# Kernel optimization log

Hardware: AMD Instinct MI355X
Metric: run time of the kernel (lower is better)

The kernel has to match this reference:

```python
import jax, jax.numpy as jnp
import numpy as np
from jax import lax

B, T, EPROJS, DUNITS, ATT_DIM = 32, 2048, 1024, 1024, 512
ACONV_CHANS, ACONV_FILTS = 32, 15
SCALING = 2.0


def setup_inputs() -> dict:
    key = jax.random.key(0)
    ks = jax.random.split(key, 12)
    enc_hs_pad = jax.random.normal(ks[0], (B, T, EPROJS), dtype=jnp.float32)
    enc_hs_len = jax.random.randint(ks[1], (B,), T // 2, T + 1, dtype=jnp.int32)
    dec_z = jax.random.normal(ks[2], (B, DUNITS), dtype=jnp.float32)
    ap = jax.random.uniform(ks[3], (B, T), dtype=jnp.float32)
    att_prev = ap / jnp.sum(ap, axis=1, keepdims=True)  # previous attention distribution
    # parameters (PyTorch Linear: y = x @ W^T + b; stored here pre-transposed as [in, out])
    s_enc = 1.0 / np.sqrt(EPROJS)
    s_dec = 1.0 / np.sqrt(DUNITS)
    s_att = 1.0 / np.sqrt(ACONV_CHANS)
    s_g = 1.0 / np.sqrt(ATT_DIM)
    K = 2 * ACONV_FILTS + 1
    s_c = 1.0 / np.sqrt(K)
    W_enc = jax.random.uniform(ks[4], (EPROJS, ATT_DIM), jnp.float32, -s_enc, s_enc)
    b_enc = jax.random.uniform(ks[5], (ATT_DIM,), jnp.float32, -s_enc, s_enc)
    W_dec = jax.random.uniform(ks[6], (DUNITS, ATT_DIM), jnp.float32, -s_dec, s_dec)
    W_att = jax.random.uniform(ks[7], (ACONV_CHANS, ATT_DIM), jnp.float32, -s_att, s_att)
    conv_w = jax.random.uniform(ks[8], (ACONV_CHANS, 1, K), jnp.float32, -s_c, s_c)
    W_g = jax.random.uniform(ks[9], (ATT_DIM, 1), jnp.float32, -s_g, s_g)
    b_g = jax.random.uniform(ks[10], (1,), jnp.float32, -s_g, s_g)
    return {"enc_hs_pad": enc_hs_pad, "enc_hs_len": enc_hs_len, "dec_z": dec_z,
            "att_prev": att_prev, "W_enc": W_enc, "b_enc": b_enc, "W_dec": W_dec,
            "W_att": W_att, "conv_w": conv_w, "W_g": W_g, "b_g": b_g}


def reference(enc_hs_pad, enc_hs_len, dec_z, att_prev,
              W_enc, b_enc, W_dec, W_att, conv_w, W_g, b_g):
    # pre-computed encoder projection: (B, T, A)
    pre_enc = jnp.einsum('btd,da->bta', enc_hs_pad, W_enc) + b_enc
    # location conv over previous attention: (B, 1, T) -> (B, C, T), SAME padding
    pad = (conv_w.shape[-1] - 1) // 2
    att_conv = lax.conv_general_dilated(
        att_prev[:, None, :], conv_w, window_strides=(1,),
        padding=[(pad, pad)], dimension_numbers=('NCH', 'OIH', 'NCH'))
    att_c = jnp.einsum('bct,ca->bta', att_conv, W_att)       # (B, T, A)
    dec_t = (dec_z @ W_dec)[:, None, :]                       # (B, 1, A)
    # energies: (B, T)
    e = jnp.einsum('bta,ao->bt', jnp.tanh(att_c + pre_enc + dec_t), W_g) + b_g[0]
    # pad mask: True where t >= length
    mask = jnp.arange(e.shape[1])[None, :] >= enc_hs_len[:, None]
    e = jnp.where(mask, -jnp.inf, e)
    w = jax.nn.softmax(SCALING * e, axis=1)                   # (B, T)
    c = jnp.einsum('btd,bt->bd', enc_hs_pad, w)               # (B, EPROJS)
    return c, w
```

## Files before the change

### kernel.cpp

```cpp
#include <hip/hip_runtime.h>
#include <stdint.h>

#define T_LEN 2048
#define KAUG  1056
#define M_TOT 65536

typedef __attribute__((ext_vector_type(8))) short short8;
typedef __attribute__((ext_vector_type(4))) float f32x4;
typedef unsigned int u32;
typedef unsigned short u16;

__device__ __forceinline__ u16 bf16_rn(float f){
  u32 u = __builtin_bit_cast(u32, f);
  u32 r = u + 0x7fffu + ((u >> 16) & 1u);
  return (u16)(r >> 16);
}
__device__ __forceinline__ u32 pack_trunc(float lo, float hi){
  u32 a = __builtin_bit_cast(u32, lo);
  u32 b = __builtin_bit_cast(u32, hi);
  return (a >> 16) | (b & 0xffff0000u);
}

__global__ void k_build_bt(const float* __restrict__ W_enc,
                           const float* __restrict__ W_att,
                           u16* __restrict__ Bt){
  __shared__ float tile[32][33];
  int k0 = blockIdx.x * 32, n0 = blockIdx.y * 32;
  int tx = threadIdx.x & 31, ty = threadIdx.x >> 5;
  #pragma unroll
  for (int i = 0; i < 4; i++){
    int k = k0 + i*8 + ty;
    int n = n0 + tx;
    float v = (k < 1024) ? W_enc[k*512 + n] : W_att[(k-1024)*512 + n];
    tile[i*8+ty][tx] = v;
  }
  __syncthreads();
  #pragma unroll
  for (int i = 0; i < 4; i++){
    int n = n0 + i*8 + ty;
    int k = k0 + tx;
    Bt[(size_t)n*KAUG + k] = bf16_rn(tile[tx][i*8+ty]);
  }
}

__global__ void k_bias(const float* __restrict__ dec_z,
                       const float* __restrict__ W_dec,
                       const float* __restrict__ b_enc,
                       float* __restrict__ bias){
  __shared__ float red[4][64];
  int b = blockIdx.y, n0 = blockIdx.x * 64;
  int nl = threadIdx.x & 63, ks = threadIdx.x >> 6;
  int n = n0 + nl;
  const float* dz = dec_z + b*1024;
  float s = 0.f;
  #pragma unroll 4
  for (int k = ks*256; k < ks*256 + 256; k++) s += dz[k] * W_dec[k*512 + n];
  red[ks][nl] = s;
  __syncthreads();
  if (threadIdx.x < 64){
    int nn = n0 + threadIdx.x;
    bias[b*512 + nn] = b_enc[nn] + red[0][threadIdx.x] + red[1][threadIdx.x]
                     + red[2][threadIdx.x] + red[3][threadIdx.x];
  }
}

__global__ void k_conv(const float* __restrict__ att_prev,
                       const float* __restrict__ conv_w,
                       float* __restrict__ attT){
  int idx = blockIdx.x*256 + threadIdx.x;
  int c = idx & 31;
  int bt = idx >> 5;
  int b = bt >> 11, t = bt & 2047;
  const float* ap = att_prev + b*2048;
  const float* cw = conv_w + c*31;
  float s = 0.f;
  #pragma unroll
  for (int j = 0; j < 31; j++){
    int tt = t + j - 15;
    float a = (tt >= 0 && tt < 2048) ? ap[tt] : 0.f;
    s += cw[j] * a;
  }
  attT[(size_t)bt*32 + c] = s;
}

__launch_bounds__(256, 3)
__global__ void k_gemm_energy(const float* __restrict__ enc,
                              const float* __restrict__ attT,
                              const u16* __restrict__ Bt,
                              const float* __restrict__ bias,
                              const float* __restrict__ Wg,
                              float* __restrict__ ePart){
  __shared__ __align__(16) u16 Ash[2][128*32];
  __shared__ float eRed[2][128];

  const int tid  = threadIdx.x;
  const int lane = tid & 63;
  const int wid  = tid >> 6;
  const int wave_m = wid >> 1, wave_n = wid & 1;
  const int bidx = blockIdx.x;
  const int xcd  = bidx & 7;
  const int s_sq = bidx >> 3;
  const int nblk = s_sq & 3;
  const int mblk = ((s_sq >> 2) << 3) + xcd;
  const int row0 = mblk << 7;
  const int b    = mblk >> 4;

  f32x4 acc[4][4];
  #pragma unroll
  for (int i = 0; i < 4; i++)
    #pragma unroll
    for (int j = 0; j < 4; j++) acc[i][j] = (f32x4)(0.f);

  const int srow = lane >> 2;
  const int sc   = lane & 3;
  const int fr_m = lane & 15;
  const int kg   = lane >> 4;

  const u16* BtN = Bt + (size_t)(nblk*128)*KAUG;

  int r0q[2], ldsoff[2];
  #pragma unroll
  for (int q = 0; q < 2; q++){
    int r = wid*32 + q*16 + srow;
    r0q[q] = r;
    ldsoff[q] = r*32 + (sc ^ ((r >> 1) & 3))*8;
  }
  int aroff[4];
  #pragma unroll
  for (int mi = 0; mi < 4; mi++){
    int m = wave_m*64 + mi*16 + fr_m;
    aroff[mi] = m*32 + (kg ^ ((m >> 1) & 3))*8;
  }
  int bnrow[4];
  #pragma unroll
  for (int ni = 0; ni < 4; ni++)
    bnrow[ni] = wave_n*64 + ni*16 + fr_m;

  auto LOADA = [&](int t, f32x4* ra){
    const float* base; size_t rstr;
    if (t < 32){ base = enc + (size_t)row0*1024 + t*32; rstr = 1024; }
    else       { base = attT + (size_t)row0*32;         rstr = 32;  }
    #pragma unroll
    for (int q = 0; q < 2; q++){
      const float* p = base + (size_t)r0q[q]*rstr + sc*8;
      ra[q*2+0] = *(const f32x4*)(p);
      ra[q*2+1] = *(const f32x4*)(p + 4);
    }
  };
  auto LOADBF = [&](int t, short8* bf){
    #pragma unroll
    for (int ni = 0; ni < 4; ni++)
      bf[ni] = *(const short8*)(BtN + (size_t)bnrow[ni]*KAUG + t*32 + kg*8);
  };
  auto WRITEA = [&](const f32x4* ra, int bi){
    #pragma unroll
    for (int q = 0; q < 2; q++){
      f32x4 lo = ra[q*2+0], hi = ra[q*2+1];
      union { u32 u[4]; short8 v; } cv;
      cv.u[0] = pack_trunc(lo.x, lo.y);
      cv.u[1] = pack_trunc(lo.z, lo.w);
      cv.u[2] = pack_trunc(hi.x, hi.y);
      cv.u[3] = pack_trunc(hi.z, hi.w);
      *(short8*)&Ash[bi][ldsoff[q]] = cv.v;
    }
  };
  auto COMPUTE = [&](int bi, const short8* bf){
    const u16* Ab = &Ash[bi][0];
    #pragma unroll
    for (int mi = 0; mi < 4; mi++){
      short8 af = *(const short8*)(Ab + aroff[mi]);
      #pragma unroll
      for (int ni = 0; ni < 4; ni++)
        acc[mi][ni] = __builtin_amdgcn_mfma_f32_16x16x32_bf16(af, bf[ni], acc[mi][ni], 0, 0, 0);
    }
  };

  f32x4 raA[4], raB[4];
  short8 bfA[4], bfB[4];
  LOADA(0, raA); LOADBF(0, bfA);

  #pragma unroll 1
  for (int i = 0; i < 16; i++){
    int kk = 2*i;
    LOADA(kk+1, raB); LOADBF(kk+1, bfB);
    WRITEA(raA, 0);
    asm volatile("s_waitcnt lgkmcnt(0)" ::: "memory");
    __builtin_amdgcn_s_barrier();
    asm volatile("" ::: "memory");
    COMPUTE(0, bfA);
    LOADA(kk+2, raA); LOADBF(kk+2, bfA);
    WRITEA(raB, 1);
    asm volatile("s_waitcnt lgkmcnt(0)" ::: "memory");
    __builtin_amdgcn_s_barrier();
    asm volatile("" ::: "memory");
    COMPUTE(1, bfB);
  }
  WRITEA(raA, 0);
  asm volatile("s_waitcnt lgkmcnt(0)" ::: "memory");
  __builtin_amdgcn_s_barrier();
  asm volatile("" ::: "memory");
  COMPUTE(0, bfA);

  float wg[4], bs[4];
  #pragma unroll
  for (int ni = 0; ni < 4; ni++){
    int ng = nblk*128 + wave_n*64 + ni*16 + fr_m;
    wg[ni] = Wg[ng];
    bs[ni] = bias[b*512 + ng];
  }
  #pragma unroll
  for (int mi = 0; mi < 4; mi++){
    #pragma unroll
    for (int reg = 0; reg < 4; reg++){
      float s = 0.f;
      #pragma unroll
      for (int ni = 0; ni < 4; ni++){
        float v  = acc[mi][ni][reg] + bs[ni];
        float e2 = __expf(2.f * v);
        float th = 1.f - 2.f/(e2 + 1.f);
        s += wg[ni] * th;
      }
      s += __shfl_xor(s, 1);
      s += __shfl_xor(s, 2);
      s += __shfl_xor(s, 4);
      s += __shfl_xor(s, 8);
      if (fr_m == 0){
        int rowl = wave_m*64 + mi*16 + kg*4 + reg;
        eRed[wave_n][rowl] = s;
      }
    }
  }
  __syncthreads();
  if (tid < 128)
    ePart[(size_t)nblk*M_TOT + row0 + tid] = eRed[0][tid] + eRed[1][tid];
}

__global__ void k_softmax(const float* __restrict__ ePart,
                          const int* __restrict__ lens,
                          float* __restrict__ wout){
  int b = blockIdx.x, tid = threadIdx.x;
  int lane = tid & 63, wid = tid >> 6;
  int len = lens[b];
  __shared__ float red[4];
  float x[8]; float m = -3.0e38f;
  #pragma unroll
  for (int i = 0; i < 8; i++){
    int t = tid + i*256;
    int idx = b*2048 + t;
    float e = ePart[idx] + ePart[M_TOT + idx] + ePart[2*M_TOT + idx] + ePart[3*M_TOT + idx];
    float xx = (t < len) ? 2.0f*e : -3.0e38f;
    x[i] = xx; m = fmaxf(m, xx);
  }
  #pragma unroll
  for (int o = 1; o < 64; o <<= 1) m = fmaxf(m, __shfl_xor(m, o));
  if (lane == 0) red[wid] = m;
  __syncthreads();
  m = fmaxf(fmaxf(red[0], red[1]), fmaxf(red[2], red[3]));
  float s = 0.f;
  #pragma unroll
  for (int i = 0; i < 8; i++){
    float ex = (x[i] > -1.0e38f) ? __expf(x[i] - m) : 0.f;
    x[i] = ex; s += ex;
  }
  #pragma unroll
  for (int o = 1; o < 64; o <<= 1) s += __shfl_xor(s, o);
  __syncthreads();
  if (lane == 0) red[wid] = s;
  __syncthreads();
  s = red[0] + red[1] + red[2] + red[3];
  float inv = 1.0f / s;
  #pragma unroll
  for (int i = 0; i < 8; i++){
    int t = tid + i*256;
    wout[b*2048 + t] = x[i]*inv;
  }
}

__global__ void k_ctx_partial(const float* __restrict__ enc,
                              const float* __restrict__ w,
                              float* __restrict__ cPart){
  int dc = blockIdx.x, tc = blockIdx.y, b = blockIdx.z;
  int d = dc*256 + threadIdx.x;
  const float* ep = enc + ((size_t)(b*2048 + tc*256))*1024 + d;
  const float* wp = w + b*2048 + tc*256;
  float s0 = 0, s1 = 0, s2 = 0, s3 = 0;
  #pragma unroll 2
  for (int t = 0; t < 256; t += 4){
    s0 += wp[t+0] * ep[(size_t)(t+0)*1024];
    s1 += wp[t+1] * ep[(size_t)(t+1)*1024];
    s2 += wp[t+2] * ep[(size_t)(t+2)*1024];
    s3 += wp[t+3] * ep[(size_t)(t+3)*1024];
  }
  cPart[((size_t)tc*32 + b)*1024 + d] = (s0 + s1) + (s2 + s3);
}

__global__ void k_ctx_reduce(const float* __restrict__ cPart, float* __restrict__ cOut){
  int idx = blockIdx.x*256 + threadIdx.x;
  float s = 0.f;
  #pragma unroll
  for (int tc = 0; tc < 8; tc++) s += cPart[tc*32768 + idx];
  cOut[idx] = s;
}

extern "C" void kernel_launch(void* const* d_in, const int* in_sizes, int n_in,
                              void* d_out, int out_size, void* d_ws, size_t ws_size,
                              hipStream_t stream){
  (void)in_sizes; (void)n_in; (void)out_size; (void)ws_size;
  const float* enc    = (const float*)d_in[0];
  const int*   lens   = (const int*)  d_in[1];
  const float* dec_z  = (const float*)d_in[2];
  const float* att_p  = (const float*)d_in[3];
  const float* W_enc  = (const float*)d_in[4];
  const float* b_enc  = (const float*)d_in[5];
  const float* W_dec  = (const float*)d_in[6];
  const float* W_att  = (const float*)d_in[7];
  const float* conv_w = (const float*)d_in[8];
  const float* W_g    = (const float*)d_in[9];

  char* ws = (char*)d_ws;
  u16*   Bt    = (u16*)  (ws);
  float* attT  = (float*)(ws + 1081344);
  float* bias  = (float*)(ws + 1081344 + 8388608);
  float* ePart = (float*)(ws + 1081344 + 8388608 + 65536);
  float* cPart = (float*)(ws + 1081344 + 8388608 + 65536 + 1048576);

  float* c_out = (float*)d_out;
  float* w_out = c_out + 32*1024;

  hipLaunchKernelGGL(k_build_bt,    dim3(33,16),  dim3(256), 0, stream, W_enc, W_att, Bt);
  hipLaunchKernelGGL(k_bias,        dim3(8,32),   dim3(256), 0, stream, dec_z, W_dec, b_enc, bias);
  hipLaunchKernelGGL(k_conv,        dim3(8192),   dim3(256), 0, stream, att_p, conv_w, attT);
  hipLaunchKernelGGL(k_gemm_energy, dim3(2048),   dim3(256), 0, stream, enc, attT, Bt, bias, W_g, ePart);
  hipLaunchKernelGGL(k_softmax,     dim3(32),     dim3(256), 0, stream, ePart, lens, w_out);
  hipLaunchKernelGGL(k_ctx_partial, dim3(4,8,32), dim3(256), 0, stream, enc, w_out, cPart);
  hipLaunchKernelGGL(k_ctx_reduce,  dim3(128),    dim3(256), 0, stream, cPart, c_out);
}
```

Baseline: 601.9 us.

## Pre-pack encoder to bf16 tiles and stage A via direct global-to-LDS loads

Adds a pre-pass that converts the fp32 encoder into bf16 in a tile-major layout, with the conv output written into the same packed buffer. The GEMM then stages A tiles with global_load_lds into a triple-buffered LDS ring, which drops the register round trip and the in-kernel conversion, and it raises occupancy to 4 blocks. The cost is an extra full pass that reads 256MB and writes 128MB of bf16, plus a large workspace requirement. A fallback path keeps the old kernels when the workspace is too small.

```diff
diff --git a/kernel.cpp b/kernel.cpp
--- a/kernel.cpp
+++ b/kernel.cpp
@@ -4,6 +4,7 @@
 #define T_LEN 2048
 #define KAUG  1056
 #define M_TOT 65536
+#define TILE_U16 135168
 
 typedef __attribute__((ext_vector_type(8))) short short8;
 typedef __attribute__((ext_vector_type(4))) float f32x4;
@@ -15,10 +16,18 @@
   u32 r = u + 0x7fffu + ((u >> 16) & 1u);
   return (u16)(r >> 16);
 }
+__device__ __forceinline__ u32 pack_rn(float lo, float hi){
+  return (u32)bf16_rn(lo) | ((u32)bf16_rn(hi) << 16);
+}
 __device__ __forceinline__ u32 pack_trunc(float lo, float hi){
   u32 a = __builtin_bit_cast(u32, lo);
   u32 b = __builtin_bit_cast(u32, hi);
   return (a >> 16) | (b & 0xffff0000u);
+}
+__device__ __forceinline__ void lds_load16(const void* g, void* l){
+  __builtin_amdgcn_global_load_lds(
+      (const __attribute__((address_space(1))) u32*)g,
+      (__attribute__((address_space(3))) u32*)l, 16, 0, 0);
 }
 
 __global__ void k_build_bt(const float* __restrict__ W_enc,
@@ -64,9 +73,26 @@
   }
 }
 
-__global__ void k_conv(const float* __restrict__ att_prev,
-                       const float* __restrict__ conv_w,
-                       float* __restrict__ attT){
+__global__ void k_pack(const float* __restrict__ enc, u16* __restrict__ Apack){
+  int e = blockIdx.x*256 + threadIdx.x;
+  int row   = e >> 7;
+  int chunk = e & 127;
+  const float* src = enc + (size_t)row*1024 + chunk*8;
+  f32x4 a = *(const f32x4*)src;
+  f32x4 b = *(const f32x4*)(src + 4);
+  union { u32 u[4]; short8 v; } cv;
+  cv.u[0] = pack_rn(a.x, a.y);
+  cv.u[1] = pack_rn(a.z, a.w);
+  cv.u[2] = pack_rn(b.x, b.y);
+  cv.u[3] = pack_rn(b.z, b.w);
+  int mblk = row >> 7, t = chunk >> 2, kin = (chunk & 3)*8;
+  u16* d = Apack + (size_t)mblk*TILE_U16 + t*4096 + (row & 127)*32 + kin;
+  *(short8*)d = cv.v;
+}
+
+__global__ void k_conv_p(const float* __restrict__ att_prev,
+                         const float* __restrict__ conv_w,
+                         u16* __restrict__ Apack){
   int idx = blockIdx.x*256 + threadIdx.x;
   int c = idx & 31;
   int bt = idx >> 5;
@@ -80,17 +106,17 @@
     float a = (tt >= 0 && tt < 2048) ? ap[tt] : 0.f;
     s += cw[j] * a;
   }
-  attT[(size_t)bt*32 + c] = s;
-}
-
-__launch_bounds__(256, 3)
-__global__ void k_gemm_energy(const float* __restrict__ enc,
-                              const float* __restrict__ attT,
-                              const u16* __restrict__ Bt,
-                              const float* __restrict__ bias,
-                              const float* __restrict__ Wg,
-                              float* __restrict__ ePart){
-  __shared__ __align__(16) u16 Ash[2][128*32];
+  int mblk = bt >> 7;
+  Apack[(size_t)mblk*TILE_U16 + 32*4096 + (bt & 127)*32 + c] = bf16_rn(s);
+}
+
+__launch_bounds__(256, 4)
+__global__ void k_gemm_energy_p(const u16* __restrict__ Apack,
+                                const u16* __restrict__ Bt,
+                                const float* __restrict__ bias,
+                                const float* __restrict__ Wg,
+                                float* __restrict__ ePart){
+  __shared__ __align__(16) u16 Ash[3][4096];
   __shared__ float eRed[2][128];
 
   const int tid  = threadIdx.x;
@@ -111,95 +137,76 @@
     #pragma unroll
     for (int j = 0; j < 4; j++) acc[i][j] = (f32x4)(0.f);
 
-  const int srow = lane >> 2;
-  const int sc   = lane & 3;
   const int fr_m = lane & 15;
   const int kg   = lane >> 4;
 
-  const u16* BtN = Bt + (size_t)(nblk*128)*KAUG;
-
-  int r0q[2], ldsoff[2];
-  #pragma unroll
-  for (int q = 0; q < 2; q++){
-    int r = wid*32 + q*16 + srow;
-    r0q[q] = r;
-    ldsoff[q] = r*32 + (sc ^ ((r >> 1) & 3))*8;
-  }
+  const u16* Atile = Apack + (size_t)mblk*TILE_U16;
+  const u16* asrc  = Atile + (wid*2)*512 + lane*8;
+  const u16* BtN   = Bt + (size_t)(nblk*128)*KAUG;
+
+  const u16* bptr0 = BtN + (size_t)(wave_n*64 +  0 + fr_m)*KAUG + kg*8;
+  const u16* bptr1 = BtN + (size_t)(wave_n*64 + 16 + fr_m)*KAUG + kg*8;
+  const u16* bptr2 = BtN + (size_t)(wave_n*64 + 32 + fr_m)*KAUG + kg*8;
+  const u16* bptr3 = BtN + (size_t)(wave_n*64 + 48 + fr_m)*KAUG + kg*8;
+
   int aroff[4];
   #pragma unroll
   for (int mi = 0; mi < 4; mi++){
     int m = wave_m*64 + mi*16 + fr_m;
-    aroff[mi] = m*32 + (kg ^ ((m >> 1) & 3))*8;
-  }
-  int bnrow[4];
-  #pragma unroll
-  for (int ni = 0; ni < 4; ni++)
-    bnrow[ni] = wave_n*64 + ni*16 + fr_m;
-
-  auto LOADA = [&](int t, f32x4* ra){
-    const float* base; size_t rstr;
-    if (t < 32){ base = enc + (size_t)row0*1024 + t*32; rstr = 1024; }
-    else       { base = attT + (size_t)row0*32;         rstr = 32;  }
-    #pragma unroll
-    for (int q = 0; q < 2; q++){
-      const float* p = base + (size_t)r0q[q]*rstr + sc*8;
-      ra[q*2+0] = *(const f32x4*)(p);
-      ra[q*2+1] = *(const f32x4*)(p + 4);
-    }
+    aroff[mi] = m*32 + kg*8;
+  }
+
+  auto STAGE = [&](int t, int bufi){
+    const u16* s0 = asrc + t*4096;
+    lds_load16(s0,       &Ash[bufi][(wid*2 + 0)*512]);
+    lds_load16(s0 + 512, &Ash[bufi][(wid*2 + 1)*512]);
   };
   auto LOADBF = [&](int t, short8* bf){
-    #pragma unroll
-    for (int ni = 0; ni < 4; ni++)
-      bf[ni] = *(const short8*)(BtN + (size_t)bnrow[ni]*KAUG + t*32 + kg*8);
-  };
-  auto WRITEA = [&](const f32x4* ra, int bi){
-    #pragma unroll
-    for (int q = 0; q < 2; q++){
-      f32x4 lo = ra[q*2+0], hi = ra[q*2+1];
-      union { u32 u[4]; short8 v; } cv;
-      cv.u[0] = pack_trunc(lo.x, lo.y);
-      cv.u[1] = pack_trunc(lo.z, lo.w);
-      cv.u[2] = pack_trunc(hi.x, hi.y);
-      cv.u[3] = pack_trunc(hi.z, hi.w);
-      *(short8*)&Ash[bi][ldsoff[q]] = cv.v;
-    }
-  };
-  auto COMPUTE = [&](int bi, const short8* bf){
-    const u16* Ab = &Ash[bi][0];
+    bf[0] = *(const short8*)(bptr0 + t*32);
+    bf[1] = *(const short8*)(bptr1 + t*32);
+    bf[2] = *(const short8*)(bptr2 + t*32);
+    bf[3] = *(const short8*)(bptr3 + t*32);
+  };
+  auto COMPUTE = [&](int bufi, const short8* bf){
     #pragma unroll
     for (int mi = 0; mi < 4; mi++){
-      short8 af = *(const short8*)(Ab + aroff[mi]);
+      short8 af = *(const short8*)&Ash[bufi][aroff[mi]];
       #pragma unroll
       for (int ni = 0; ni < 4; ni++)
         acc[mi][ni] = __builtin_amdgcn_mfma_f32_16x16x32_bf16(af, bf[ni], acc[mi][ni], 0, 0, 0);
     }
   };
 
-  f32x4 raA[4], raB[4];
   short8 bfA[4], bfB[4];
-  LOADA(0, raA); LOADBF(0, bfA);
-
+  STAGE(0, 0);
+  LOADBF(0, bfA);
+  STAGE(1, 1);
+
+  int bE = 0;
   #pragma unroll 1
   for (int i = 0; i < 16; i++){
-    int kk = 2*i;
-    LOADA(kk+1, raB); LOADBF(kk+1, bfB);
-    WRITEA(raA, 0);
-    asm volatile("s_waitcnt lgkmcnt(0)" ::: "memory");
+    int t  = 2*i;
+    int bO = (bE == 2) ? 0 : bE + 1;
+    int sE = (bO == 2) ? 0 : bO + 1;
+    int sO = bE;
+    LOADBF(t+1, bfB);
+    asm volatile("s_waitcnt vmcnt(6)" ::: "memory");
     __builtin_amdgcn_s_barrier();
     asm volatile("" ::: "memory");
-    COMPUTE(0, bfA);
-    LOADA(kk+2, raA); LOADBF(kk+2, bfA);
-    WRITEA(raB, 1);
-    asm volatile("s_waitcnt lgkmcnt(0)" ::: "memory");
+    if (t < 31) STAGE(t+2, sE);
+    COMPUTE(bE, bfA);
+    LOADBF(t+2, bfA);
+    asm volatile("s_waitcnt vmcnt(6)" ::: "memory");
     __builtin_amdgcn_s_barrier();
     asm volatile("" ::: "memory");
-    COMPUTE(1, bfB);
-  }
-  WRITEA(raA, 0);
-  asm volatile("s_waitcnt lgkmcnt(0)" ::: "memory");
+    if (t+1 < 31) STAGE(t+3, sO);
+    COMPUTE(bO, bfB);
+    bE = sE;
+  }
+  asm volatile("s_waitcnt vmcnt(0)" ::: "memory");
   __builtin_amdgcn_s_barrier();
   asm volatile("" ::: "memory");
-  COMPUTE(0, bfA);
+  COMPUTE(bE, bfA);
 
   float wg[4], bs[4];
   #pragma unroll
@@ -235,6 +242,168 @@
     ePart[(size_t)nblk*M_TOT + row0 + tid] = eRed[0][tid] + eRed[1][tid];
 }
 
+__global__ void k_conv_f(const float* __restrict__ att_prev,
+                         const float* __restrict__ conv_w,
+                         float* __restrict__ attT){
+  int idx = blockIdx.x*256 + threadIdx.x;
+  int c = idx & 31;
+  int bt = idx >> 5;
+  int b = bt >> 11, t = bt & 2047;
+  const float* ap = att_prev + b*2048;
+  const float* cw = conv_w + c*31;
+  float s = 0.f;
+  #pragma unroll
+  for (int j = 0; j < 31; j++){
+    int tt = t + j - 15;
+    float a = (tt >= 0 && tt < 2048) ? ap[tt] : 0.f;
+    s += cw[j] * a;
+  }
+  attT[(size_t)bt*32 + c] = s;
+}
+
+__launch_bounds__(256, 3)
+__global__ void k_gemm_energy_f(const float* __restrict__ enc,
+                                const float* __restrict__ attT,
+                                const u16* __restrict__ Bt,
+                                const float* __restrict__ bias,
+                                const float* __restrict__ Wg,
+                                float* __restrict__ ePart){
+  __shared__ __align__(16) u16 Ash[2][128*32];
+  __shared__ float eRed[2][128];
+  const int tid  = threadIdx.x;
+  const int lane = tid & 63;
+  const int wid  = tid >> 6;
+  const int wave_m = wid >> 1, wave_n = wid & 1;
+  const int bidx = blockIdx.x;
+  const int xcd  = bidx & 7;
+  const int s_sq = bidx >> 3;
+  const int nblk = s_sq & 3;
+  const int mblk = ((s_sq >> 2) << 3) + xcd;
+  const int row0 = mblk << 7;
+  const int b    = mblk >> 4;
+  f32x4 acc[4][4];
+  #pragma unroll
+  for (int i = 0; i < 4; i++)
+    #pragma unroll
+    for (int j = 0; j < 4; j++) acc[i][j] = (f32x4)(0.f);
+  const int srow = lane >> 2;
+  const int sc   = lane & 3;
+  const int fr_m = lane & 15;
+  const int kg   = lane >> 4;
+  const u16* BtN = Bt + (size_t)(nblk*128)*KAUG;
+  int r0q[2], ldsoff[2];
+  #pragma unroll
+  for (int q = 0; q < 2; q++){
+    int r = wid*32 + q*16 + srow;
+    r0q[q] = r;
+    ldsoff[q] = r*32 + (sc ^ ((r >> 1) & 3))*8;
+  }
+  int aroff[4];
+  #pragma unroll
+  for (int mi = 0; mi < 4; mi++){
+    int m = wave_m*64 + mi*16 + fr_m;
+    aroff[mi] = m*32 + (kg ^ ((m >> 1) & 3))*8;
+  }
+  int bnrow[4];
+  #pragma unroll
+  for (int ni = 0; ni < 4; ni++)
+    bnrow[ni] = wave_n*64 + ni*16 + fr_m;
+  auto LOADA = [&](int t, f32x4* ra){
+    const float* base; size_t rstr;
+    if (t < 32){ base = enc + (size_t)row0*1024 + t*32; rstr = 1024; }
+    else       { base = attT + (size_t)row0*32;         rstr = 32;  }
+    #pragma unroll
+    for (int q = 0; q < 2; q++){
+      const float* p = base + (size_t)r0q[q]*rstr + sc*8;
+      ra[q*2+0] = *(const f32x4*)(p);
+      ra[q*2+1] = *(const f32x4*)(p + 4);
+    }
+  };
+  auto LOADBF = [&](int t, short8* bf){
+    #pragma unroll
+    for (int ni = 0; ni < 4; ni++)
+      bf[ni] = *(const short8*)(BtN + (size_t)bnrow[ni]*KAUG + t*32 + kg*8);
+  };
+  auto WRITEA = [&](const f32x4* ra, int bi){
+    #pragma unroll
+    for (int q = 0; q < 2; q++){
+      f32x4 lo = ra[q*2+0], hi = ra[q*2+1];
+      union { u32 u[4]; short8 v; } cv;
+      cv.u[0] = pack_trunc(lo.x, lo.y);
+      cv.u[1] = pack_trunc(lo.z, lo.w);
+      cv.u[2] = pack_trunc(hi.x, hi.y);
+      cv.u[3] = pack_trunc(hi.z, hi.w);
+      *(short8*)&Ash[bi][ldsoff[q]] = cv.v;
+    }
+  };
+  auto COMPUTE = [&](int bi, const short8* bf){
+    const u16* Ab = &Ash[bi][0];
+    #pragma unroll
+    for (int mi = 0; mi < 4; mi++){
+      short8 af = *(const short8*)(Ab + aroff[mi]);
+      #pragma unroll
+      for (int ni = 0; ni < 4; ni++)
+        acc[mi][ni] = __builtin_amdgcn_mfma_f32_16x16x32_bf16(af, bf[ni], acc[mi][ni], 0, 0, 0);
+    }
+  };
+  f32x4 raA[4], raB[4];
+  short8 bfA[4], bfB[4];
+  LOADA(0, raA); LOADBF(0, bfA);
+  #pragma unroll 1
+  for (int i = 0; i < 16; i++){
+    int kk = 2*i;
+    LOADA(kk+1, raB); LOADBF(kk+1, bfB);
+    WRITEA(raA, 0);
+    asm volatile("s_waitcnt lgkmcnt(0)" ::: "memory");
+    __builtin_amdgcn_s_barrier();
+    asm volatile("" ::: "memory");
+    COMPUTE(0, bfA);
+    LOADA(kk+2, raA); LOADBF(kk+2, bfA);
+    WRITEA(raB, 1);
+    asm volatile("s_waitcnt lgkmcnt(0)" ::: "memory");
+    __builtin_amdgcn_s_barrier();
+    asm volatile("" ::: "memory");
+    COMPUTE(1, bfB);
+  }
+  WRITEA(raA, 0);
+  asm volatile("s_waitcnt lgkmcnt(0)" ::: "memory");
+  __builtin_amdgcn_s_barrier();
+  asm volatile("" ::: "memory");
+  COMPUTE(0, bfA);
+  float wg[4], bs[4];
+  #pragma unroll
+  for (int ni = 0; ni < 4; ni++){
+    int ng = nblk*128 + wave_n*64 + ni*16 + fr_m;
+    wg[ni] = Wg[ng];
+    bs[ni] = bias[b*512 + ng];
+  }
+  #pragma unroll
+  for (int mi = 0; mi < 4; mi++){
+    #pragma unroll
+    for (int reg = 0; reg < 4; reg++){
+      float s = 0.f;
+      #pragma unroll
+      for (int ni = 0; ni < 4; ni++){
+        float v  = acc[mi][ni][reg] + bs[ni];
+        float e2 = __expf(2.f * v);
+        float th = 1.f - 2.f/(e2 + 1.f);
+        s += wg[ni] * th;
+      }
+      s += __shfl_xor(s, 1);
+      s += __shfl_xor(s, 2);
+      s += __shfl_xor(s, 4);
+      s += __shfl_xor(s, 8);
+      if (fr_m == 0){
+        int rowl = wave_m*64 + mi*16 + kg*4 + reg;
+        eRed[wave_n][rowl] = s;
+      }
+    }
+  }
+  __syncthreads();
+  if (tid < 128)
+    ePart[(size_t)nblk*M_TOT + row0 + tid] = eRed[0][tid] + eRed[1][tid];
+}
+
 __global__ void k_softmax(const float* __restrict__ ePart,
                           const int* __restrict__ lens,
                           float* __restrict__ wout){
@@ -305,7 +474,7 @@
 extern "C" void kernel_launch(void* const* d_in, const int* in_sizes, int n_in,
                               void* d_out, int out_size, void* d_ws, size_t ws_size,
                               hipStream_t stream){
-  (void)in_sizes; (void)n_in; (void)out_size; (void)ws_size;
+  (void)in_sizes; (void)n_in; (void)out_size;
   const float* enc    = (const float*)d_in[0];
   const int*   lens   = (const int*)  d_in[1];
   const float* dec_z  = (const float*)d_in[2];
@@ -317,21 +486,39 @@
   const float* conv_w = (const float*)d_in[8];
   const float* W_g    = (const float*)d_in[9];
 
-  char* ws = (char*)d_ws;
-  u16*   Bt    = (u16*)  (ws);
-  float* attT  = (float*)(ws + 1081344);
-  float* bias  = (float*)(ws + 1081344 + 8388608);
-  float* ePart = (float*)(ws + 1081344 + 8388608 + 65536);
-  float* cPart = (float*)(ws + 1081344 + 8388608 + 65536 + 1048576);
-
   float* c_out = (float*)d_out;
   float* w_out = c_out + 32*1024;
 
-  hipLaunchKernelGGL(k_build_bt,    dim3(33,16),  dim3(256), 0, stream, W_enc, W_att, Bt);
-  hipLaunchKernelGGL(k_bias,        dim3(8,32),   dim3(256), 0, stream, dec_z, W_dec, b_enc, bias);
-  hipLaunchKernelGGL(k_conv,        dim3(8192),   dim3(256), 0, stream, att_p, conv_w, attT);
-  hipLaunchKernelGGL(k_gemm_energy, dim3(2048),   dim3(256), 0, stream, enc, attT, Bt, bias, W_g, ePart);
-  hipLaunchKernelGGL(k_softmax,     dim3(32),     dim3(256), 0, stream, ePart, lens, w_out);
-  hipLaunchKernelGGL(k_ctx_partial, dim3(4,8,32), dim3(256), 0, stream, enc, w_out, cPart);
-  hipLaunchKernelGGL(k_ctx_reduce,  dim3(128),    dim3(256), 0, stream, cPart, c_out);
-}
+  char* ws = (char*)d_ws;
+
+  if (ws_size >= 141656064ull){
+    u16*   Bt    = (u16*)  (ws);
+    float* bias  = (float*)(ws + 1081344);
+    float* ePart = (float*)(ws + 1146880);
+    float* cPart = (float*)(ws + 2195456);
+    u16*   Apack = (u16*)  (ws + 3244032);
+
+    hipLaunchKernelGGL(k_build_bt,      dim3(33,16),  dim3(256), 0, stream, W_enc, W_att, Bt);
+    hipLaunchKernelGGL(k_bias,          dim3(8,32),   dim3(256), 0, stream, dec_z, W_dec, b_enc, bias);
+    hipLaunchKernelGGL(k_pack,          dim3(32768),  dim3(256), 0, stream, enc, Apack);
+    hipLaunchKernelGGL(k_conv_p,        dim3(8192),   dim3(256), 0, stream, att_p, conv_w, Apack);
+    hipLaunchKernelGGL(k_gemm_energy_p, dim3(2048),   dim3(256), 0, stream, Apack, Bt, bias, W_g, ePart);
+    hipLaunchKernelGGL(k_softmax,       dim3(32),     dim3(256), 0, stream, ePart, lens, w_out);
+    hipLaunchKernelGGL(k_ctx_partial,   dim3(4,8,32), dim3(256), 0, stream, enc, w_out, cPart);
+    hipLaunchKernelGGL(k_ctx_reduce,    dim3(128),    dim3(256), 0, stream, cPart, c_out);
+  } else {
+    u16*   Bt    = (u16*)  (ws);
+    float* attT  = (float*)(ws + 1081344);
+    float* bias  = (float*)(ws + 1081344 + 8388608);
+    float* ePart = (float*)(ws + 1081344 + 8388608 + 65536);
+    float* cPart = (float*)(ws + 1081344 + 8388608 + 65536 + 1048576);
+
+    hipLaunchKernelGGL(k_build_bt,      dim3(33,16),  dim3(256), 0, stream, W_enc, W_att, Bt);
+    hipLaunchKernelGGL(k_bias,          dim3(8,32),   dim3(256), 0, stream, dec_z, W_dec, b_enc, bias);
+    hipLaunchKernelGGL(k_conv_f,        dim3(8192),   dim3(256), 0, stream, att_p, conv_w, attT);
+    hipLaunchKernelGGL(k_gemm_energy_f, dim3(2048),   dim3(256), 0, stream, enc, attT, Bt, bias, W_g, ePart);
+    hipLaunchKernelGGL(k_softmax,       dim3(32),     dim3(256), 0, stream, ePart, lens, w_out);
+    hipLaunchKernelGGL(k_ctx_partial,   dim3(4,8,32), dim3(256), 0, stream, enc, w_out, cPart);
+    hipLaunchKernelGGL(k_ctx_reduce,    dim3(128),    dim3(256), 0, stream, cPart, c_out);
+  }
+}
```

After: 634.4 us. +5.4%, slower.

## Enlarge energy GEMM tile to 256 rows with 8 waves and 64-wide K steps

Applied to the files above, without the earlier changes.

The fused projection+energy GEMM now uses 512-thread blocks computing 256x128 tiles with a 2x4 wave layout. Each pipeline step covers K=64, with the padded augmented K raised to 1088. Each thread loads a contiguous 32-float span of the fp32 A row, and MFMA bursts are wrapped in s_setprio. The aim is better A/B reuse, fewer barriers per K, and more coalesced A loads, at the cost of more registers and LDS per block and some zero-padded K work.

```diff
diff --git a/kernel.cpp b/kernel.cpp
--- a/kernel.cpp
+++ b/kernel.cpp
@@ -1,8 +1,7 @@
 #include <hip/hip_runtime.h>
 #include <stdint.h>
 
-#define T_LEN 2048
-#define KAUG  1056
+#define KAUG2 1088
 #define M_TOT 65536
 
 typedef __attribute__((ext_vector_type(8))) short short8;
@@ -31,7 +30,8 @@
   for (int i = 0; i < 4; i++){
     int k = k0 + i*8 + ty;
     int n = n0 + tx;
-    float v = (k < 1024) ? W_enc[k*512 + n] : W_att[(k-1024)*512 + n];
+    float v = (k < 1024) ? W_enc[k*512 + n]
+            : (k < 1056) ? W_att[(k-1024)*512 + n] : 0.f;
     tile[i*8+ty][tx] = v;
   }
   __syncthreads();
@@ -39,7 +39,7 @@
   for (int i = 0; i < 4; i++){
     int n = n0 + i*8 + ty;
     int k = k0 + tx;
-    Bt[(size_t)n*KAUG + k] = bf16_rn(tile[tx][i*8+ty]);
+    Bt[(size_t)n*KAUG2 + k] = bf16_rn(tile[tx][i*8+ty]);
   }
 }
 
@@ -83,138 +83,147 @@
   attT[(size_t)bt*32 + c] = s;
 }
 
-__launch_bounds__(256, 3)
-__global__ void k_gemm_energy(const float* __restrict__ enc,
-                              const float* __restrict__ attT,
-                              const u16* __restrict__ Bt,
-                              const float* __restrict__ bias,
-                              const float* __restrict__ Wg,
-                              float* __restrict__ ePart){
-  __shared__ __align__(16) u16 Ash[2][128*32];
-  __shared__ float eRed[2][128];
+__global__ __launch_bounds__(512, 2)
+void k_gemm_energy8(const float* __restrict__ enc,
+                    const float* __restrict__ attT,
+                    const u16* __restrict__ Bt,
+                    const float* __restrict__ bias,
+                    const float* __restrict__ Wg,
+                    float* __restrict__ ePart){
+  __shared__ __align__(16) u16 Ash[2][16384];
+  __shared__ float eRed[4][256];
 
   const int tid  = threadIdx.x;
   const int lane = tid & 63;
   const int wid  = tid >> 6;
-  const int wave_m = wid >> 1, wave_n = wid & 1;
+  const int wave_m = wid >> 2;
+  const int wave_n = wid & 3;
+
   const int bidx = blockIdx.x;
   const int xcd  = bidx & 7;
   const int s_sq = bidx >> 3;
   const int nblk = s_sq & 3;
   const int mblk = ((s_sq >> 2) << 3) + xcd;
-  const int row0 = mblk << 7;
-  const int b    = mblk >> 4;
-
-  f32x4 acc[4][4];
-  #pragma unroll
-  for (int i = 0; i < 4; i++)
-    #pragma unroll
-    for (int j = 0; j < 4; j++) acc[i][j] = (f32x4)(0.f);
-
-  const int srow = lane >> 2;
-  const int sc   = lane & 3;
+  const int row0 = mblk << 8;
+  const int b    = mblk >> 3;
+
+  f32x4 acc[8][2];
+  #pragma unroll
+  for (int i = 0; i < 8; i++){ acc[i][0] = (f32x4)(0.f); acc[i][1] = (f32x4)(0.f); }
+
   const int fr_m = lane & 15;
   const int kg   = lane >> 4;
 
-  const u16* BtN = Bt + (size_t)(nblk*128)*KAUG;
-
-  int r0q[2], ldsoff[2];
-  #pragma unroll
-  for (int q = 0; q < 2; q++){
-    int r = wid*32 + q*16 + srow;
-    r0q[q] = r;
-    ldsoff[q] = r*32 + (sc ^ ((r >> 1) & 3))*8;
-  }
-  int aroff[4];
-  #pragma unroll
-  for (int mi = 0; mi < 4; mi++){
-    int m = wave_m*64 + mi*16 + fr_m;
+  const int r  = tid >> 1;
+  const int kh = tid & 1;
+  const float* aEnc = enc  + (size_t)(row0 + r)*1024 + kh*32;
+  const float* aAtt = attT + (size_t)(row0 + r)*32;
+  int woff[4];
+  #pragma unroll
+  for (int c = 0; c < 4; c++)
+    woff[c] = (kh*256 + r)*32 + (c ^ ((r >> 1) & 3))*8;
+
+  int aroff[8];
+  #pragma unroll
+  for (int mi = 0; mi < 8; mi++){
+    int m = wave_m*128 + mi*16 + fr_m;
     aroff[mi] = m*32 + (kg ^ ((m >> 1) & 3))*8;
   }
-  int bnrow[4];
-  #pragma unroll
-  for (int ni = 0; ni < 4; ni++)
-    bnrow[ni] = wave_n*64 + ni*16 + fr_m;
-
-  auto LOADA = [&](int t, f32x4* ra){
-    const float* base; size_t rstr;
-    if (t < 32){ base = enc + (size_t)row0*1024 + t*32; rstr = 1024; }
-    else       { base = attT + (size_t)row0*32;         rstr = 32;  }
-    #pragma unroll
-    for (int q = 0; q < 2; q++){
-      const float* p = base + (size_t)r0q[q]*rstr + sc*8;
-      ra[q*2+0] = *(const f32x4*)(p);
-      ra[q*2+1] = *(const f32x4*)(p + 4);
-    }
+
+  const u16* bp0 = Bt + (size_t)(nblk*128 + wave_n*32 +      fr_m)*KAUG2 + kg*8;
+  const u16* bp1 = Bt + (size_t)(nblk*128 + wave_n*32 + 16 + fr_m)*KAUG2 + kg*8;
+
+  f32x4 ast[8];
+  short8 bE[4], bO[4];
+
+  auto LOADA = [&](int pp){
+    const float* p = (pp < 16) ? (aEnc + pp*64) : aAtt;
+    #pragma unroll
+    for (int q = 0; q < 8; q++) ast[q] = *(const f32x4*)(p + q*4);
   };
-  auto LOADBF = [&](int t, short8* bf){
-    #pragma unroll
-    for (int ni = 0; ni < 4; ni++)
-      bf[ni] = *(const short8*)(BtN + (size_t)bnrow[ni]*KAUG + t*32 + kg*8);
+  auto LOADB = [&](int pp, short8* bf){
+    int o = pp*64;
+    bf[0] = *(const short8*)(bp0 + o);
+    bf[1] = *(const short8*)(bp1 + o);
+    bf[2] = *(const short8*)(bp0 + o + 32);
+    bf[3] = *(const short8*)(bp1 + o + 32);
   };
-  auto WRITEA = [&](const f32x4* ra, int bi){
-    #pragma unroll
-    for (int q = 0; q < 2; q++){
-      f32x4 lo = ra[q*2+0], hi = ra[q*2+1];
+  auto PACK_WRITE = [&](int buf){
+    #pragma unroll
+    for (int c = 0; c < 4; c++){
+      f32x4 lo = ast[2*c], hi = ast[2*c+1];
       union { u32 u[4]; short8 v; } cv;
       cv.u[0] = pack_trunc(lo.x, lo.y);
       cv.u[1] = pack_trunc(lo.z, lo.w);
       cv.u[2] = pack_trunc(hi.x, hi.y);
       cv.u[3] = pack_trunc(hi.z, hi.w);
-      *(short8*)&Ash[bi][ldsoff[q]] = cv.v;
+      *(short8*)&Ash[buf][woff[c]] = cv.v;
     }
   };
-  auto COMPUTE = [&](int bi, const short8* bf){
-    const u16* Ab = &Ash[bi][0];
-    #pragma unroll
-    for (int mi = 0; mi < 4; mi++){
-      short8 af = *(const short8*)(Ab + aroff[mi]);
-      #pragma unroll
-      for (int ni = 0; ni < 4; ni++)
-        acc[mi][ni] = __builtin_amdgcn_mfma_f32_16x16x32_bf16(af, bf[ni], acc[mi][ni], 0, 0, 0);
+  auto COMPUTE = [&](int buf, const short8* bf){
+    const u16* A0 = &Ash[buf][0];
+    short8 af[8];
+    #pragma unroll
+    for (int mi = 0; mi < 8; mi++) af[mi] = *(const short8*)(A0 + aroff[mi]);
+    __builtin_amdgcn_s_setprio(1);
+    #pragma unroll
+    for (int mi = 0; mi < 8; mi++){
+      acc[mi][0] = __builtin_amdgcn_mfma_f32_16x16x32_bf16(af[mi], bf[0], acc[mi][0], 0, 0, 0);
+      acc[mi][1] = __builtin_amdgcn_mfma_f32_16x16x32_bf16(af[mi], bf[1], acc[mi][1], 0, 0, 0);
     }
+    __builtin_amdgcn_s_setprio(0);
+    #pragma unroll
+    for (int mi = 0; mi < 8; mi++) af[mi] = *(const short8*)(A0 + 8192 + aroff[mi]);
+    __builtin_amdgcn_s_setprio(1);
+    #pragma unroll
+    for (int mi = 0; mi < 8; mi++){
+      acc[mi][0] = __builtin_amdgcn_mfma_f32_16x16x32_bf16(af[mi], bf[2], acc[mi][0], 0, 0, 0);
+      acc[mi][1] = __builtin_amdgcn_mfma_f32_16x16x32_bf16(af[mi], bf[3], acc[mi][1], 0, 0, 0);
+    }
+    __builtin_amdgcn_s_setprio(0);
   };
 
-  f32x4 raA[4], raB[4];
-  short8 bfA[4], bfB[4];
-  LOADA(0, raA); LOADBF(0, bfA);
+  LOADA(0); LOADB(0, bE);
+  asm volatile("s_waitcnt vmcnt(4)" ::: "memory");
+  PACK_WRITE(0);
+  asm volatile("s_waitcnt lgkmcnt(0)" ::: "memory");
+  __builtin_amdgcn_s_barrier();
+  asm volatile("" ::: "memory");
 
   #pragma unroll 1
-  for (int i = 0; i < 16; i++){
-    int kk = 2*i;
-    LOADA(kk+1, raB); LOADBF(kk+1, bfB);
-    WRITEA(raA, 0);
+  for (int i = 0; i < 8; i++){
+    int p = 2*i;
+    LOADA(p+1); LOADB(p+1, bO);
+    COMPUTE(0, bE);
+    asm volatile("s_waitcnt vmcnt(4)" ::: "memory");
+    PACK_WRITE(1);
     asm volatile("s_waitcnt lgkmcnt(0)" ::: "memory");
     __builtin_amdgcn_s_barrier();
     asm volatile("" ::: "memory");
-    COMPUTE(0, bfA);
-    LOADA(kk+2, raA); LOADBF(kk+2, bfA);
-    WRITEA(raB, 1);
+    LOADA(p+2); LOADB(p+2, bE);
+    COMPUTE(1, bO);
+    asm volatile("s_waitcnt vmcnt(4)" ::: "memory");
+    PACK_WRITE(0);
     asm volatile("s_waitcnt lgkmcnt(0)" ::: "memory");
     __builtin_amdgcn_s_barrier();
     asm volatile("" ::: "memory");
-    COMPUTE(1, bfB);
-  }
-  WRITEA(raA, 0);
-  asm volatile("s_waitcnt lgkmcnt(0)" ::: "memory");
-  __builtin_amdgcn_s_barrier();
-  asm volatile("" ::: "memory");
-  COMPUTE(0, bfA);
-
-  float wg[4], bs[4];
-  #pragma unroll
-  for (int ni = 0; ni < 4; ni++){
-    int ng = nblk*128 + wave_n*64 + ni*16 + fr_m;
+  }
+  COMPUTE(0, bE);
+
+  float wg[2], bs[2];
+  #pragma unroll
+  for (int ni = 0; ni < 2; ni++){
+    int ng = nblk*128 + wave_n*32 + ni*16 + fr_m;
     wg[ni] = Wg[ng];
     bs[ni] = bias[b*512 + ng];
   }
   #pragma unroll
-  for (int mi = 0; mi < 4; mi++){
+  for (int mi = 0; mi < 8; mi++){
     #pragma unroll
     for (int reg = 0; reg < 4; reg++){
       float s = 0.f;
       #pragma unroll
-      for (int ni = 0; ni < 4; ni++){
+      for (int ni = 0; ni < 2; ni++){
         float v  = acc[mi][ni][reg] + bs[ni];
         float e2 = __expf(2.f * v);
         float th = 1.f - 2.f/(e2 + 1.f);
@@ -224,15 +233,14 @@
       s += __shfl_xor(s, 2);
       s += __shfl_xor(s, 4);
       s += __shfl_xor(s, 8);
-      if (fr_m == 0){
-        int rowl = wave_m*64 + mi*16 + kg*4 + reg;
-        eRed[wave_n][rowl] = s;
-      }
+      if (fr_m == 0)
+        eRed[wave_n][wave_m*128 + mi*16 + kg*4 + reg] = s;
     }
   }
   __syncthreads();
-  if (tid < 128)
-    ePart[(size_t)nblk*M_TOT + row0 + tid] = eRed[0][tid] + eRed[1][tid];
+  if (tid < 256)
+    ePart[(size_t)nblk*M_TOT + row0 + tid]
+        = eRed[0][tid] + eRed[1][tid] + eRed[2][tid] + eRed[3][tid];
 }
 
 __global__ void k_softmax(const float* __restrict__ ePart,
@@ -319,18 +327,18 @@
 
   char* ws = (char*)d_ws;
   u16*   Bt    = (u16*)  (ws);
-  float* attT  = (float*)(ws + 1081344);
-  float* bias  = (float*)(ws + 1081344 + 8388608);
-  float* ePart = (float*)(ws + 1081344 + 8388608 + 65536);
-  float* cPart = (float*)(ws + 1081344 + 8388608 + 65536 + 1048576);
+  float* attT  = (float*)(ws + 1114112);
+  float* bias  = (float*)(ws + 9502720);
+  float* ePart = (float*)(ws + 9568256);
+  float* cPart = (float*)(ws + 10616832);
 
   float* c_out = (float*)d_out;
   float* w_out = c_out + 32*1024;
 
-  hipLaunchKernelGGL(k_build_bt,    dim3(33,16),  dim3(256), 0, stream, W_enc, W_att, Bt);
+  hipLaunchKernelGGL(k_build_bt,    dim3(34,16),  dim3(256), 0, stream, W_enc, W_att, Bt);
   hipLaunchKernelGGL(k_bias,        dim3(8,32),   dim3(256), 0, stream, dec_z, W_dec, b_enc, bias);
   hipLaunchKernelGGL(k_conv,        dim3(8192),   dim3(256), 0, stream, att_p, conv_w, attT);
-  hipLaunchKernelGGL(k_gemm_energy, dim3(2048),   dim3(256), 0, stream, enc, attT, Bt, bias, W_g, ePart);
+  hipLaunchKernelGGL(k_gemm_energy8,dim3(1024),   dim3(512), 0, stream, enc, attT, Bt, bias, W_g, ePart);
   hipLaunchKernelGGL(k_softmax,     dim3(32),     dim3(256), 0, stream, ePart, lens, w_out);
   hipLaunchKernelGGL(k_ctx_partial, dim3(4,8,32), dim3(256), 0, stream, enc, w_out, cPart);
   hipLaunchKernelGGL(k_ctx_reduce,  dim3(128),    dim3(256), 0, stream, cPart, c_out);
```

Measured after the change: 671.1 us. +11.5%, slower.
